# Optimization experiments

Measured on AMD Instinct MI355X. Metric: run time of the kernel, lower is better.

Reference implementation:

```python
import jax, jax.numpy as jnp
import numpy as np

VOCAB, D_MODEL, N_STATE, H_HEADS, LAYERS = 64, 512, 32, 16, 4
EXPAND = 2
D_INNER = EXPAND * D_MODEL          # 1024
P_HEAD = D_INNER // H_HEADS         # 64
CONV_DIM = D_INNER + 2 * N_STATE    # x, B, C share the depthwise conv
K_CONV = 4
D_IN_PROJ = 2 * D_INNER + 2 * N_STATE + H_HEADS  # z, x, B, C, dt
BATCH, SEQ = 4, 1024
EPS = 1e-5


def rmsnorm(x, w):
    return x * jax.lax.rsqrt(jnp.mean(x * x, axis=-1, keepdims=True) + EPS) * w


def silu(x):
    return x * jax.nn.sigmoid(x)


def causal_depthwise_conv(x, w, b):
    # x: [B,L,C], w: [C,K], b: [C]; causal (left) padding, depthwise groups
    xt = jnp.transpose(x, (0, 2, 1))  # [B,C,L]
    out = jax.lax.conv_general_dilated(xt, w[:, None, :], (1,), [(K_CONV - 1, 0)], feature_group_count=w.shape[0])
    return jnp.transpose(out, (0, 2, 1)) + b


def ssd(xh, dt, A, Bm, Cm, Dp):
    # Mamba2 SSD recurrence. xh [B,L,H,P], dt [B,L,H], A [H], Bm/Cm [B,L,N], Dp [H]
    dA = jnp.exp(dt * A)              # decay per (batch, step, head)
    dtx = dt[..., None] * xh          # [B,L,H,P]

    def step(h, inp):
        dA_t, dtx_t, B_t, C_t = inp
        # h: [B,H,P,N]
        h = dA_t[:, :, None, None] * h + dtx_t[..., None] * B_t[:, None, None, :]
        y = jnp.einsum('bhpn,bn->bhp', h, C_t)
        return h, y

    h0 = jnp.zeros((xh.shape[0], H_HEADS, P_HEAD, N_STATE), xh.dtype)
    _, ys = jax.lax.scan(step, h0, (jnp.moveaxis(dA, 1, 0), jnp.moveaxis(dtx, 1, 0), jnp.moveaxis(Bm, 1, 0), jnp.moveaxis(Cm, 1, 0)))
    return jnp.moveaxis(ys, 0, 1) + xh * Dp[None, None, :, None]


def mamba_block(x, norm_w, W_in, b_in, conv_w, conv_b, dt_bias, A_log, Dp, gnorm_w, W_out, b_out):
    res = x
    u = rmsnorm(x, norm_w)
    zxbcdt = u @ W_in + b_in                                # [B,L,D_IN_PROJ]
    z = zxbcdt[..., :D_INNER]
    xBC = zxbcdt[..., D_INNER:D_INNER + CONV_DIM]
    dt = zxbcdt[..., D_INNER + CONV_DIM:]                   # [B,L,H]
    xBC = silu(causal_depthwise_conv(xBC, conv_w, conv_b))
    xc = xBC[..., :D_INNER]
    Bm = xBC[..., D_INNER:D_INNER + N_STATE]
    Cm = xBC[..., D_INNER + N_STATE:]
    dt = jax.nn.softplus(dt + dt_bias)
    xh = xc.reshape(xc.shape[0], xc.shape[1], H_HEADS, P_HEAD)
    y = ssd(xh, dt, -jnp.exp(A_log), Bm, Cm, Dp)
    y = y.reshape(y.shape[0], y.shape[1], D_INNER)
    y = rmsnorm(y * silu(z), gnorm_w)                       # gated RMSNorm
    return res + y @ W_out + b_out


def forward(input_tokens, emb, norm_w, W_in, b_in, conv_w, conv_b, dt_bias, A_log, D_param, gnorm_w, W_out, b_out, head_w, head_b):
    h = emb[input_tokens]
    for i in range(LAYERS):
        h = mamba_block(h, norm_w[i], W_in[i], b_in[i], conv_w[i], conv_b[i], dt_bias[i], A_log[i], D_param[i], gnorm_w[i], W_out[i], b_out[i])
    return h @ head_w + head_b


def setup_inputs() -> dict:
    key = jax.random.key(0)
    ks = jax.random.split(key, 8)
    s = 0.02
    return {
        'input_tokens': jax.random.randint(ks[0], (BATCH, SEQ), 0, VOCAB),
        'emb': jax.random.normal(ks[1], (VOCAB, D_MODEL), jnp.float32) * s,
        'norm_w': jnp.ones((LAYERS, D_MODEL), jnp.float32),
        'W_in': jax.random.normal(ks[2], (LAYERS, D_MODEL, D_IN_PROJ), jnp.float32) * s,
        'b_in': jnp.zeros((LAYERS, D_IN_PROJ), jnp.float32),
        'conv_w': jax.random.normal(ks[3], (LAYERS, CONV_DIM, K_CONV), jnp.float32) * 0.1,
        'conv_b': jnp.zeros((LAYERS, CONV_DIM), jnp.float32),
        'dt_bias': jnp.tile(jnp.log(jnp.expm1(jnp.linspace(0.001, 0.1, H_HEADS, dtype=jnp.float32))), (LAYERS, 1)),
        'A_log': jnp.tile(jnp.log(jnp.arange(1, H_HEADS + 1, dtype=jnp.float32)), (LAYERS, 1)),
        'D_param': jnp.ones((LAYERS, H_HEADS), jnp.float32),
        'gnorm_w': jnp.ones((LAYERS, D_INNER), jnp.float32),
        'W_out': jax.random.normal(ks[4], (LAYERS, D_INNER, D_MODEL), jnp.float32) * s,
        'b_out': jnp.zeros((LAYERS, D_MODEL), jnp.float32),
        'head_w': jax.random.normal(ks[5], (D_MODEL, VOCAB), jnp.float32) * s,
        'head_b': jnp.zeros((VOCAB,), jnp.float32),
    }


def reference(input_tokens, emb, norm_w, W_in, b_in, conv_w, conv_b, dt_bias, A_log, D_param, gnorm_w, W_out, b_out, head_w, head_b):
    return forward(input_tokens, emb, norm_w, W_in, b_in, conv_w, conv_b, dt_bias, A_log, D_param, gnorm_w, W_out, b_out, head_w, head_b)
```

## Files before the change

kernel.cpp:

```cpp
#include <hip/hip_runtime.h>
#include <hip/hip_bf16.h>

#define VOCAB     64
#define D_MODEL   512
#define N_STATE   32
#define H_HEADS   16
#define LAYERS    4
#define D_INNER   1024
#define P_HEAD    64
#define CONV_DIM  1088
#define K_CONV    4
#define D_IN_PROJ 2128
#define NPAD_IN   2176
#define NPAD_HEAD 64
#define BATCH     4
#define SEQ       1024
#define NTOK      (BATCH*SEQ)
#define EPS       1e-5f
#define CL        64
#define NC        (SEQ/CL)
#define PSTR      80

typedef __bf16 bf16x8 __attribute__((ext_vector_type(8)));
typedef float  f32x4  __attribute__((ext_vector_type(4)));

__device__ __forceinline__ float sigmoidf_(float x) { return 1.f / (1.f + __expf(-x)); }
__device__ __forceinline__ float softplusf_(float x) { return (x > 20.f) ? x : log1pf(__expf(x)); }

__device__ __forceinline__ void gload_lds16(const void* g, void* l) {
  __builtin_amdgcn_global_load_lds((const __attribute__((address_space(1))) void*)g,
                                   (__attribute__((address_space(3))) void*)l,
                                   16, 0, 0);
}

__device__ __forceinline__ int xcd_lin() {
  return (blockIdx.x & 7) * ((int)gridDim.x >> 3) + ((int)blockIdx.x >> 3);
}

__global__ __launch_bounds__(256) void prep_kernel(
    const float* __restrict__ W_in, const float* __restrict__ W_out,
    const float* __restrict__ head_w,
    const float* __restrict__ norm_w, const float* __restrict__ gnorm_w,
    __bf16* __restrict__ WtIn, __bf16* __restrict__ WtOut, __bf16* __restrict__ WtHead,
    const int* __restrict__ tok, const float* __restrict__ emb,
    float* __restrict__ h, __bf16* __restrict__ hbf) {
  int b = blockIdx.x;
  if (b >= 6432) {
    int eb = b - 6432;
    int wv = threadIdx.x >> 6, lane = threadIdx.x & 63;
    int tokid = eb * 4 + wv;
    const float* er = emb + (size_t)tok[tokid] * D_MODEL;
    f32x4 v0 = *(const f32x4*)(er + lane * 8);
    f32x4 v1 = *(const f32x4*)(er + lane * 8 + 4);
    float* hr = h + (size_t)tokid * D_MODEL;
    *(f32x4*)(hr + lane * 8) = v0;
    *(f32x4*)(hr + lane * 8 + 4) = v1;
    bf16x8 o8;
    #pragma unroll
    for (int k = 0; k < 4; k++) { o8[k] = (__bf16)v0[k]; o8[4 + k] = (__bf16)v1[k]; }
    *(bf16x8*)(hbf + (size_t)tokid * D_MODEL + lane * 8) = o8;
    return;
  }
  const float* W; const float* fold; __bf16* Wt; int K, N, Npad, bx, by;
  if (b < 4352) {
    int z = b / 1088, r = b % 1088;
    bx = r % 68; by = r / 68;
    W = W_in + (size_t)z * D_MODEL * D_IN_PROJ;
    fold = norm_w + (size_t)z * D_MODEL;
    Wt = WtIn + (size_t)z * NPAD_IN * D_MODEL;
    K = D_MODEL; N = D_IN_PROJ; Npad = NPAD_IN;
  } else if (b < 6400) {
    int r = b - 4352; int z = r / 512; r %= 512;
    bx = r % 16; by = r / 16;
    W = W_out + (size_t)z * D_INNER * D_MODEL;
    fold = gnorm_w + (size_t)z * D_INNER;
    Wt = WtOut + (size_t)z * D_MODEL * D_INNER;
    K = D_INNER; N = D_MODEL; Npad = D_MODEL;
  } else {
    int r = b - 6400;
    bx = r % 2; by = r / 2;
    W = head_w; fold = nullptr; Wt = WtHead;
    K = D_MODEL; N = VOCAB; Npad = NPAD_HEAD;
  }
  __shared__ float T[32][33];
  int n0 = bx * 32, k0 = by * 32;
  int tx = threadIdx.x & 31, ty = threadIdx.x >> 5;
  #pragma unroll
  for (int i = 0; i < 4; i++) {
    int n = n0 + tx;
    T[ty + i * 8][tx] = (n < N) ? W[(size_t)(k0 + ty + i * 8) * N + n] : 0.f;
  }
  __syncthreads();
  float fs = fold ? fold[k0 + tx] : 1.f;
  #pragma unroll
  for (int i = 0; i < 4; i++)
    Wt[(size_t)(n0 + ty + i * 8) * K + k0 + tx] = (__bf16)(T[tx][ty + i * 8] * fs);
}

#define TK 64
__global__ __launch_bounds__(256) void gemm64_kernel(
    const __bf16* __restrict__ A, const __bf16* __restrict__ Bt,
    const float* __restrict__ bias, const float* __restrict__ res,
    float* __restrict__ C, __bf16* __restrict__ Cbf,
    float inv_norm_dim, int nbx, int K, int N, int ldc) {
  __shared__ __bf16 As[3][64 * TK];
  __shared__ __bf16 Bs[3][32 * TK];
  int tid = threadIdx.x;
  int lane = tid & 63, wave = tid >> 6;
  int wm = wave >> 1, wn = wave & 1;
  int q = lane >> 4, l16 = lane & 15;
  int lin = xcd_lin();
  int bx = lin % nbx, by = lin / nbx;
  size_t row0 = (size_t)by * 64;
  int col0 = bx * 32;
  const __bf16* Ab = A + row0 * K;
  const __bf16* Bb = Bt + (size_t)col0 * K;

  auto stage = [&](int buf, int kk) {
    #pragma unroll
    for (int r = 0; r < 2; r++) {
      int lin2 = r * 256 + tid;
      gload_lds16(Ab + (size_t)(lin2 >> 3) * K + kk + (lin2 & 7) * 8, &As[buf][lin2 * 8]);
    }
    {
      int lin2 = tid;
      gload_lds16(Bb + (size_t)(lin2 >> 3) * K + kk + (lin2 & 7) * 8, &Bs[buf][lin2 * 8]);
    }
  };

  f32x4 acc[2];
  acc[0] = (f32x4){0.f, 0.f, 0.f, 0.f};
  acc[1] = (f32x4){0.f, 0.f, 0.f, 0.f};
  float ssqa[2] = {0.f, 0.f};

  int niter = K / TK;
  stage(0, 0);
  if (niter > 1) stage(1, TK);
  int bi = 0;
  for (int i = 0; i < niter; i++) {
    if (i + 2 < niter) {
      stage((bi + 2) % 3, (i + 2) * TK);
      asm volatile("s_waitcnt vmcnt(6)" ::: "memory");
    } else if (i + 1 < niter) {
      asm volatile("s_waitcnt vmcnt(3)" ::: "memory");
    } else {
      asm volatile("s_waitcnt vmcnt(0)" ::: "memory");
    }
    __builtin_amdgcn_s_barrier();
    #pragma unroll
    for (int ks = 0; ks < 2; ks++) {
      bf16x8 af[2], bfv;
      #pragma unroll
      for (int ii = 0; ii < 2; ii++) {
        af[ii] = *(const bf16x8*)(&As[bi][(wm * 32 + ii * 16 + l16) * TK + ks * 32 + q * 8]);
        #pragma unroll
        for (int k = 0; k < 8; k++) { float v = (float)af[ii][k]; ssqa[ii] += v * v; }
      }
      bfv = *(const bf16x8*)(&Bs[bi][(wn * 16 + l16) * TK + ks * 32 + q * 8]);
      #pragma unroll
      for (int ii = 0; ii < 2; ii++)
        acc[ii] = __builtin_amdgcn_mfma_f32_16x16x32_bf16(af[ii], bfv, acc[ii], 0, 0, 0);
    }
    __builtin_amdgcn_s_barrier();
    bi = (bi + 1) % 3;
  }

  #pragma unroll
  for (int i = 0; i < 2; i++) {
    ssqa[i] += __shfl_xor(ssqa[i], 16);
    ssqa[i] += __shfl_xor(ssqa[i], 32);
  }
  #pragma unroll
  for (int i = 0; i < 2; i++) {
    #pragma unroll
    for (int rr = 0; rr < 4; rr++) {
      size_t mrow = row0 + wm * 32 + i * 16 + q * 4 + rr;
      float sq = __shfl(ssqa[i], q * 4 + rr);
      float sc = (inv_norm_dim > 0.f) ? rsqrtf(sq * inv_norm_dim + EPS) : 1.f;
      int col = col0 + wn * 16 + l16;
      if (col < N) {
        size_t off = mrow * (size_t)ldc + col;
        float v = acc[i][rr] * sc + (bias ? bias[col] : 0.f);
        if (res) v += res[off];
        if (C)   C[off] = v;
        if (Cbf) Cbf[off] = (__bf16)v;
      }
    }
  }
}

__global__ __launch_bounds__(256) void gemm_in_kernel(
    const __bf16* __restrict__ A, const __bf16* __restrict__ Bt,
    const float* __restrict__ bias, __bf16* __restrict__ Cbf,
    int nbx, int K, int N, int ldc) {
  __shared__ __bf16 As[64 * TK];
  __shared__ __bf16 Bs[2][128 * TK];
  int tid = threadIdx.x;
  int lane = tid & 63, wave = tid >> 6;
  int wm = wave >> 1, wn = wave & 1;
  int q = lane >> 4, l16 = lane & 15;
  int lin = xcd_lin();
  int bx = lin % nbx, by = lin / nbx;
  size_t row0 = (size_t)by * 64;
  int col0 = bx * 128;
  const __bf16* Ab = A + row0 * K;
  const __bf16* Bb = Bt + (size_t)col0 * K;

  auto stageA = [&](int kk) {
    #pragma unroll
    for (int r = 0; r < 2; r++) {
      int lin2 = r * 256 + tid;
      gload_lds16(Ab + (size_t)(lin2 >> 3) * K + kk + (lin2 & 7) * 8, As + lin2 * 8);
    }
  };
  auto stageB = [&](int buf, int kk) {
    #pragma unroll
    for (int r = 0; r < 4; r++) {
      int lin2 = r * 256 + tid;
      gload_lds16(Bb + (size_t)(lin2 >> 3) * K + kk + (lin2 & 7) * 8, &Bs[buf][lin2 * 8]);
    }
  };

  f32x4 acc[2][4];
  #pragma unroll
  for (int i = 0; i < 2; i++)
    #pragma unroll
    for (int j = 0; j < 4; j++) acc[i][j] = (f32x4){0.f, 0.f, 0.f, 0.f};
  float ssqa[2] = {0.f, 0.f};

  stageA(0);
  stageB(0, 0);
  int cur = 0;
  for (int k0 = 0; k0 < K; k0 += TK) {
    if (k0 + TK < K) {
      stageB(cur ^ 1, k0 + TK);
      asm volatile("s_waitcnt vmcnt(4)" ::: "memory");
    } else {
      asm volatile("s_waitcnt vmcnt(0)" ::: "memory");
    }
    __builtin_amdgcn_s_barrier();
    #pragma unroll
    for (int ks = 0; ks < 2; ks++) {
      bf16x8 af[2], bfv[4];
      #pragma unroll
      for (int i = 0; i < 2; i++) {
        af[i] = *(const bf16x8*)(&As[(wm * 32 + i * 16 + l16) * TK + ks * 32 + q * 8]);
        #pragma unroll
        for (int k = 0; k < 8; k++) { float v = (float)af[i][k]; ssqa[i] += v * v; }
      }
      #pragma unroll
      for (int j = 0; j < 4; j++)
        bfv[j] = *(const bf16x8*)(&Bs[cur][(wn * 64 + j * 16 + l16) * TK + ks * 32 + q * 8]);
      #pragma unroll
      for (int i = 0; i < 2; i++)
        #pragma unroll
        for (int j = 0; j < 4; j++)
          acc[i][j] = __builtin_amdgcn_mfma_f32_16x16x32_bf16(af[i], bfv[j], acc[i][j], 0, 0, 0);
    }
    __builtin_amdgcn_s_barrier();
    if (k0 + TK < K) stageA(k0 + TK);
    cur ^= 1;
  }

  #pragma unroll
  for (int i = 0; i < 2; i++) {
    ssqa[i] += __shfl_xor(ssqa[i], 16);
    ssqa[i] += __shfl_xor(ssqa[i], 32);
  }
  __bf16* Cs = (__bf16*)Bs;
  const int CST = 136;
  float bvj[4];
  #pragma unroll
  for (int j = 0; j < 4; j++) {
    int colj = col0 + wn * 64 + j * 16 + l16;
    bvj[j] = (colj < N) ? bias[colj] : 0.f;
  }
  #pragma unroll
  for (int i = 0; i < 2; i++) {
    #pragma unroll
    for (int rr = 0; rr < 4; rr++) {
      int rloc = wm * 32 + i * 16 + q * 4 + rr;
      float sq = __shfl(ssqa[i], q * 4 + rr);
      float sc = rsqrtf(sq * (1.f / D_MODEL) + EPS);
      #pragma unroll
      for (int j = 0; j < 4; j++)
        Cs[rloc * CST + wn * 64 + j * 16 + l16] = (__bf16)(acc[i][j][rr] * sc + bvj[j]);
    }
  }
  __syncthreads();
  #pragma unroll
  for (int s = 0; s < 2; s++) {
    int idx = s * 256 + tid;
    int row = idx >> 3, c0 = (idx & 7) * 16;
    if (col0 + c0 < N) {
      bf16x8 v0 = *(const bf16x8*)(&Cs[row * CST + c0]);
      bf16x8 v1 = *(const bf16x8*)(&Cs[row * CST + c0 + 8]);
      __bf16* dst = Cbf + (row0 + row) * (size_t)ldc + col0 + c0;
      *(bf16x8*)dst = v0;
      *(bf16x8*)(dst + 8) = v1;
    }
  }
}

__device__ __forceinline__ void wave0_dt_cumsum(
    const __bf16* __restrict__ zxbf, const float* __restrict__ dt_bias,
    int b, int h, int t0, int tid, float* ldt, float* lcs, float* __restrict__ dtcsg) {
  if (tid < 64) {
    float dv = (float)zxbf[((size_t)(b * SEQ + t0 + tid)) * D_IN_PROJ + 2 * D_INNER + 2 * N_STATE + h]
               + dt_bias[h];
    float dtv = softplusf_(dv);
    float cs = dtv;
    #pragma unroll
    for (int off = 1; off < 64; off <<= 1) {
      float o = __shfl_up(cs, off);
      if (tid >= off) cs += o;
    }
    ldt[tid] = dtv;
    lcs[tid] = cs;
    dtcsg[tid] = dtv;
    dtcsg[64 + tid] = cs;
  }
}

__global__ __launch_bounds__(256) void ssd_local_kernel(
    const __bf16* __restrict__ zxbf, const float* __restrict__ conv_w,
    const float* __restrict__ conv_b, const float* __restrict__ dt_bias,
    const float* __restrict__ A_log,
    float* __restrict__ Slocal, float* __restrict__ dAprod,
    __bf16* __restrict__ convx, __bf16* __restrict__ convbc, float* __restrict__ dtcs) {
  int blk = xcd_lin();
  int c = blk % NC;
  int h = (blk / NC) % H_HEADS;
  int b = blk / (NC * H_HEADS);
  int tid = threadIdx.x;
  int lane = tid & 63, wave = tid >> 6;
  int q = lane >> 4, l16 = lane & 15;
  int t0 = c * CL;
  float A = -__expf(A_log[h]);
  __shared__ __bf16 rawbuf[2 * 68 * 64];
  __shared__ __bf16 lxT[64][PSTR];
  __shared__ __bf16 lBTw[32][PSTR];
  __shared__ float ldt[64], lcs[64];
  __bf16* rawx = rawbuf;
  __bf16* rawBC = rawbuf + 68 * 64;
  for (int i = tid; i < 68 * 8; i += 256) {
    int r = i >> 3, c0 = (i & 7) * 8;
    int gr = t0 - 3 + r;
    bf16x8 vx, vbc;
    #pragma unroll
    for (int k = 0; k < 8; k++) { vx[k] = (__bf16)0.f; vbc[k] = (__bf16)0.f; }
    if (gr >= 0) {
      const __bf16* rowp = zxbf + ((size_t)(b * SEQ + gr)) * D_IN_PROJ;
      vx  = *(const bf16x8*)(rowp + D_INNER + h * 64 + c0);
      vbc = *(const bf16x8*)(rowp + 2 * D_INNER + c0);
    }
    *(bf16x8*)(rawx + r * 64 + c0)  = vx;
    *(bf16x8*)(rawBC + r * 64 + c0) = vbc;
  }
  wave0_dt_cumsum(zxbf, dt_bias, b, h, t0, tid, ldt, lcs, dtcs + (size_t)blk * 128);
  __syncthreads();
  float cs63 = lcs[63];
  __bf16* xg  = convx  + (size_t)blk * (64 * PSTR);
  __bf16* bcg = convbc + (size_t)blk * 4096;
  {
    int p = tid & 63;
    const float* w = conv_w + (h * 64 + p) * K_CONV;
    float w0 = w[0], w1 = w[1], w2 = w[2], w3 = w[3];
    float cb = conv_b[h * 64 + p];
    for (int i = tid; i < CL * 64; i += 256) {
      int t = i >> 6;
      float a = cb + w0 * (float)rawx[t * 64 + p] + w1 * (float)rawx[(t + 1) * 64 + p]
                   + w2 * (float)rawx[(t + 2) * 64 + p] + w3 * (float)rawx[(t + 3) * 64 + p];
      lxT[p][t] = (__bf16)(a * sigmoidf_(a));
    }
  }
  {
    int col = tid & 63;
    const float* w = conv_w + (D_INNER + col) * K_CONV;
    float w0 = w[0], w1 = w[1], w2 = w[2], w3 = w[3];
    float cb = conv_b[D_INNER + col];
    for (int i = tid; i < CL * 64; i += 256) {
      int t = i >> 6;
      float a = cb + w0 * (float)rawBC[t * 64 + col] + w1 * (float)rawBC[(t + 1) * 64 + col]
                   + w2 * (float)rawBC[(t + 2) * 64 + col] + w3 * (float)rawBC[(t + 3) * 64 + col];
      float v = a * sigmoidf_(a);
      if (col < 32) {
        bcg[t * 32 + col] = (__bf16)v;
        float wt = ldt[t] * __expf(A * (cs63 - lcs[t]));
        lBTw[col][t] = (__bf16)(v * wt);
      } else {
        bcg[2048 + t * 32 + (col - 32)] = (__bf16)v;
      }
    }
  }
  __syncthreads();
  for (int i = tid; i < (64 * PSTR) / 8; i += 256)
    *(bf16x8*)(xg + i * 8) = *(const bf16x8*)(((const __bf16*)lxT) + i * 8);
  if (c < NC - 1) {
    f32x4 acc0 = (f32x4){0.f,0.f,0.f,0.f}, acc1 = (f32x4){0.f,0.f,0.f,0.f};
    #pragma unroll
    for (int kb = 0; kb < 2; kb++) {
      bf16x8 af = *(const bf16x8*)(&lxT[wave * 16 + l16][kb * 32 + q * 8]);
      bf16x8 b0 = *(const bf16x8*)(&lBTw[l16][kb * 32 + q * 8]);
      bf16x8 b1 = *(const bf16x8*)(&lBTw[l16 + 16][kb * 32 + q * 8]);
      acc0 = __builtin_amdgcn_mfma_f32_16x16x32_bf16(af, b0, acc0, 0, 0, 0);
      acc1 = __builtin_amdgcn_mfma_f32_16x16x32_bf16(af, b1, acc1, 0, 0, 0);
    }
    float* sT = (float*)rawbuf;
    #pragma unroll
    for (int rr = 0; rr < 4; rr++) {
      int p = wave * 16 + q * 4 + rr;
      sT[p * 36 + l16]      = acc0[rr];
      sT[p * 36 + l16 + 16] = acc1[rr];
    }
    int row = tid >> 2, c0 = (tid & 3) * 8;
    f32x4 a = *(const f32x4*)(sT + row * 36 + c0);
    f32x4 b2 = *(const f32x4*)(sT + row * 36 + c0 + 4);
    float* dstp = Slocal + (size_t)blk * 2048 + row * 32 + c0;
    *(f32x4*)dstp = a;
    *(f32x4*)(dstp + 4) = b2;
  }
  if (tid == 0) dAprod[blk] = __expf(A * cs63);
}

__global__ __launch_bounds__(256) void ssd_out_kernel(
    const __bf16* __restrict__ zxbf, const float* __restrict__ A_log,
    const float* __restrict__ Dp,
    const float* __restrict__ Slocal, const float* __restrict__ dAprod,
    const __bf16* __restrict__ convx, const __bf16* __restrict__ convbc,
    const float* __restrict__ dtcs, __bf16* __restrict__ gout) {
  int blk = xcd_lin();
  int c = blk % NC;
  int h = (blk / NC) % H_HEADS;
  int b = blk / (NC * H_HEADS);
  int tid = threadIdx.x;
  int lane = tid & 63, wave = tid >> 6;
  int q = lane >> 4, l16 = lane & 15;
  int t0 = c * CL;
  float A = -__expf(A_log[h]);
  float D = Dp[h];
  __shared__ __bf16 lxT[64][PSTR];
  __shared__ __bf16 pPbuf[64 * PSTR];
  __shared__ __bf16 lBC[2 * 64 * 32];
  __shared__ __bf16 lS[64][32];
  __shared__ float ldt[64], lcs[64];
  const __bf16* xg  = convx  + (size_t)blk * (64 * PSTR);
  const __bf16* bcg = convbc + (size_t)blk * 4096;
  __bf16* lB = lBC;
  __bf16* lC = lBC + 2048;
  for (int i = tid; i < (64 * PSTR) / 8; i += 256)
    gload_lds16(xg + i * 8, ((__bf16*)lxT) + i * 8);
  for (int i = tid; i < 512; i += 256)
    gload_lds16(bcg + i * 8, lBC + i * 8);
  if (tid < 64) {
    const float* dg = dtcs + (size_t)blk * 128;
    ldt[tid] = dg[tid];
    lcs[tid] = dg[64 + tid];
  }
  {
    int p = tid >> 2, n0 = (tid & 3) * 8;
    const float* sl = Slocal + (size_t)(blk - c) * 2048 + p * 32 + n0;
    const float* dab = dAprod + (blk - c);
    float st[8] = {};
    for (int j = 0; j < c; j++) {
      f32x4 a = *(const f32x4*)(sl + (size_t)j * 2048);
      f32x4 bq = *(const f32x4*)(sl + (size_t)j * 2048 + 4);
      float prj = dab[j];
      #pragma unroll
      for (int k = 0; k < 4; k++) { st[k] = prj * st[k] + a[k]; st[4 + k] = prj * st[4 + k] + bq[k]; }
    }
    #pragma unroll
    for (int k = 0; k < 8; k++) lS[p][n0 + k] = (__bf16)st[k];
  }
  __syncthreads();
  bf16x8 afC = *(const bf16x8*)(lC + (wave * 16 + l16) * 32 + q * 8);
  f32x4 accG[4], accI[4], accY[4];
  #pragma unroll
  for (int j = 0; j < 4; j++) {
    accG[j] = (f32x4){0.f,0.f,0.f,0.f};
    accI[j] = (f32x4){0.f,0.f,0.f,0.f};
    accY[j] = (f32x4){0.f,0.f,0.f,0.f};
  }
  #pragma unroll
  for (int j = 0; j < 4; j++) {
    bf16x8 bf = *(const bf16x8*)(lB + (l16 + 16 * j) * 32 + q * 8);
    accG[j] = __builtin_amdgcn_mfma_f32_16x16x32_bf16(afC, bf, accG[j], 0, 0, 0);
  }
  #pragma unroll
  for (int j = 0; j < 4; j++) {
    bf16x8 bf = *(const bf16x8*)(&lS[l16 + 16 * j][q * 8]);
    accI[j] = __builtin_amdgcn_mfma_f32_16x16x32_bf16(afC, bf, accI[j], 0, 0, 0);
  }
  __bf16* pP = pPbuf + wave * 16 * PSTR;
  #pragma unroll
  for (int j = 0; j < 4; j++) {
    int s = l16 + 16 * j;
    float css = lcs[s], dts = ldt[s];
    #pragma unroll
    for (int rr = 0; rr < 4; rr++) {
      int tl = q * 4 + rr;
      int t = wave * 16 + tl;
      float val = accG[j][rr] * __expf(A * (lcs[t] - css)) * dts;
      if (s == t) val += D;
      if (s > t) val = 0.f;
      pP[tl * PSTR + s] = (__bf16)val;
    }
  }
  #pragma unroll
  for (int kb = 0; kb < 2; kb++) {
    bf16x8 afP = *(const bf16x8*)(pP + l16 * PSTR + kb * 32 + q * 8);
    #pragma unroll
    for (int j = 0; j < 4; j++) {
      bf16x8 bf = *(const bf16x8*)(&lxT[l16 + 16 * j][kb * 32 + q * 8]);
      accY[j] = __builtin_amdgcn_mfma_f32_16x16x32_bf16(afP, bf, accY[j], 0, 0, 0);
    }
  }
  __syncthreads();
  __bf16* yT = pPbuf;
  #pragma unroll
  for (int rr = 0; rr < 4; rr++) {
    int t = wave * 16 + q * 4 + rr;
    float cumt = __expf(A * lcs[t]);
    #pragma unroll
    for (int j = 0; j < 4; j++) {
      int p = l16 + 16 * j;
      yT[t * 72 + p] = (__bf16)(accY[j][rr] + cumt * accI[j][rr]);
    }
  }
  {
    int row = tid >> 2, col0 = (tid & 3) * 16;
    bf16x8 y0 = *(const bf16x8*)(yT + row * 72 + col0);
    bf16x8 y1 = *(const bf16x8*)(yT + row * 72 + col0 + 8);
    const __bf16* zrow = zxbf + ((size_t)(b * SEQ + t0 + row)) * D_IN_PROJ + h * 64 + col0;
    bf16x8 z0 = *(const bf16x8*)zrow;
    bf16x8 z1 = *(const bf16x8*)(zrow + 8);
    bf16x8 g0, g1;
    #pragma unroll
    for (int k = 0; k < 8; k++) {
      float zz = (float)z0[k];
      g0[k] = (__bf16)((float)y0[k] * zz * sigmoidf_(zz));
    }
    #pragma unroll
    for (int k = 0; k < 8; k++) {
      float zz = (float)z1[k];
      g1[k] = (__bf16)((float)y1[k] * zz * sigmoidf_(zz));
    }
    __bf16* grow = gout + ((size_t)(b * SEQ + t0 + row)) * D_INNER + h * 64 + col0;
    *(bf16x8*)grow = g0;
    *(bf16x8*)(grow + 8) = g1;
  }
}

extern "C" void kernel_launch(void* const* d_in, const int* in_sizes, int n_in,
                              void* d_out, int out_size, void* d_ws, size_t ws_size,
                              hipStream_t stream) {
  const int*   tok     = (const int*)  d_in[0];
  const float* emb     = (const float*)d_in[1];
  const float* norm_w  = (const float*)d_in[2];
  const float* W_in    = (const float*)d_in[3];
  const float* b_in    = (const float*)d_in[4];
  const float* conv_w  = (const float*)d_in[5];
  const float* conv_b  = (const float*)d_in[6];
  const float* dt_bias = (const float*)d_in[7];
  const float* A_log   = (const float*)d_in[8];
  const float* D_par   = (const float*)d_in[9];
  const float* gnorm_w = (const float*)d_in[10];
  const float* W_out   = (const float*)d_in[11];
  const float* b_out   = (const float*)d_in[12];
  const float* head_w  = (const float*)d_in[13];
  const float* head_b  = (const float*)d_in[14];
  float* out = (float*)d_out;

  char* p = (char*)d_ws;
  auto alloc = [&](size_t bytes) { void* r = (void*)p; p += (bytes + 255) & ~(size_t)255; return r; };
  float*  h      = (float*) alloc((size_t)NTOK * D_MODEL * 4);
  float*  slocal = (float*) alloc((size_t)BATCH * H_HEADS * NC * P_HEAD * N_STATE * 4);
  float*  daprod = (float*) alloc((size_t)BATCH * H_HEADS * NC * 4);
  float*  dtcs   = (float*) alloc((size_t)1024 * 128 * 4);
  __bf16* convx  = (__bf16*)alloc((size_t)1024 * 64 * PSTR * 2);
  __bf16* convbc = (__bf16*)alloc((size_t)1024 * 4096 * 2);
  __bf16* zxbf   = (__bf16*)alloc((size_t)NTOK * D_IN_PROJ * 2);
  __bf16* gbf    = (__bf16*)alloc((size_t)NTOK * D_INNER * 2);
  __bf16* hbf    = (__bf16*)alloc((size_t)NTOK * D_MODEL * 2);
  __bf16* WtIn   = (__bf16*)alloc((size_t)LAYERS * NPAD_IN * D_MODEL * 2);
  __bf16* WtOut  = (__bf16*)alloc((size_t)LAYERS * D_MODEL * D_INNER * 2);
  __bf16* WtHead = (__bf16*)alloc((size_t)NPAD_HEAD * D_MODEL * 2);

  prep_kernel<<<6432 + NTOK / 4, 256, 0, stream>>>(
      W_in, W_out, head_w, norm_w, gnorm_w, WtIn, WtOut, WtHead,
      tok, emb, h, hbf);

  for (int l = 0; l < LAYERS; l++) {
    gemm_in_kernel<<<1088, 256, 0, stream>>>(
        hbf, WtIn + (size_t)l * NPAD_IN * D_MODEL, b_in + (size_t)l * D_IN_PROJ,
        zxbf, NPAD_IN / 128, D_MODEL, D_IN_PROJ, D_IN_PROJ);

    ssd_local_kernel<<<BATCH * H_HEADS * NC, 256, 0, stream>>>(
        zxbf, conv_w + (size_t)l * CONV_DIM * K_CONV, conv_b + (size_t)l * CONV_DIM,
        dt_bias + (size_t)l * H_HEADS, A_log + (size_t)l * H_HEADS, slocal, daprod,
        convx, convbc, dtcs);
    ssd_out_kernel<<<BATCH * H_HEADS * NC, 256, 0, stream>>>(
        zxbf, A_log + (size_t)l * H_HEADS, D_par + (size_t)l * H_HEADS,
        slocal, daprod, convx, convbc, dtcs, gbf);

    gemm64_kernel<<<1024, 256, 0, stream>>>(
        gbf, WtOut + (size_t)l * D_MODEL * D_INNER, b_out + (size_t)l * D_MODEL, h,
        h, hbf, 1.f / D_INNER, D_MODEL / 32, D_INNER, D_MODEL, D_MODEL);
  }

  gemm64_kernel<<<128, 256, 0, stream>>>(
      hbf, WtHead, head_b, nullptr, out, nullptr, 0.f, NPAD_HEAD / 32, D_MODEL, VOCAB, VOCAB);
}
```

Before: 431.9 us.

## Triple-buffer input-projection GEMM with smaller K tile and prefetch depth two

```diff
diff --git a/kernel.cpp b/kernel.cpp
--- a/kernel.cpp
+++ b/kernel.cpp
@@ -189,12 +189,13 @@
   }
 }
 
+#define TKI 32
 __global__ __launch_bounds__(256) void gemm_in_kernel(
     const __bf16* __restrict__ A, const __bf16* __restrict__ Bt,
     const float* __restrict__ bias, __bf16* __restrict__ Cbf,
     int nbx, int K, int N, int ldc) {
-  __shared__ __bf16 As[64 * TK];
-  __shared__ __bf16 Bs[2][128 * TK];
+  __shared__ __bf16 As[3][64 * TKI];
+  __shared__ __bf16 Bs[3][128 * TKI];
   int tid = threadIdx.x;
   int lane = tid & 63, wave = tid >> 6;
   int wm = wave >> 1, wn = wave & 1;
@@ -206,18 +207,14 @@
   const __bf16* Ab = A + row0 * K;
   const __bf16* Bb = Bt + (size_t)col0 * K;
 
-  auto stageA = [&](int kk) {
+  auto stage = [&](int buf, int kk) {
+    {
+      gload_lds16(Ab + (size_t)(tid >> 2) * K + kk + (tid & 3) * 8, &As[buf][tid * 8]);
+    }
     #pragma unroll
     for (int r = 0; r < 2; r++) {
       int lin2 = r * 256 + tid;
-      gload_lds16(Ab + (size_t)(lin2 >> 3) * K + kk + (lin2 & 7) * 8, As + lin2 * 8);
-    }
-  };
-  auto stageB = [&](int buf, int kk) {
-    #pragma unroll
-    for (int r = 0; r < 4; r++) {
-      int lin2 = r * 256 + tid;
-      gload_lds16(Bb + (size_t)(lin2 >> 3) * K + kk + (lin2 & 7) * 8, &Bs[buf][lin2 * 8]);
+      gload_lds16(Bb + (size_t)(lin2 >> 2) * K + kk + (lin2 & 3) * 8, &Bs[buf][lin2 * 8]);
     }
   };
 
@@ -228,38 +225,39 @@
     for (int j = 0; j < 4; j++) acc[i][j] = (f32x4){0.f, 0.f, 0.f, 0.f};
   float ssqa[2] = {0.f, 0.f};
 
-  stageA(0);
-  stageB(0, 0);
-  int cur = 0;
-  for (int k0 = 0; k0 < K; k0 += TK) {
-    if (k0 + TK < K) {
-      stageB(cur ^ 1, k0 + TK);
-      asm volatile("s_waitcnt vmcnt(4)" ::: "memory");
+  int niter = K / TKI;
+  stage(0, 0);
+  stage(1, TKI);
+  int bi = 0;
+  for (int i = 0; i < niter; i++) {
+    if (i + 2 < niter) {
+      stage((bi + 2) % 3, (i + 2) * TKI);
+      asm volatile("s_waitcnt vmcnt(6)" ::: "memory");
+    } else if (i + 1 < niter) {
+      asm volatile("s_waitcnt vmcnt(3)" ::: "memory");
     } else {
       asm volatile("s_waitcnt vmcnt(0)" ::: "memory");
     }
     __builtin_amdgcn_s_barrier();
-    #pragma unroll
-    for (int ks = 0; ks < 2; ks++) {
+    {
       bf16x8 af[2], bfv[4];
       #pragma unroll
-      for (int i = 0; i < 2; i++) {
-        af[i] = *(const bf16x8*)(&As[(wm * 32 + i * 16 + l16) * TK + ks * 32 + q * 8]);
+      for (int ii = 0; ii < 2; ii++) {
+        af[ii] = *(const bf16x8*)(&As[bi][(wm * 32 + ii * 16 + l16) * TKI + q * 8]);
         #pragma unroll
-        for (int k = 0; k < 8; k++) { float v = (float)af[i][k]; ssqa[i] += v * v; }
+        for (int k = 0; k < 8; k++) { float v = (float)af[ii][k]; ssqa[ii] += v * v; }
       }
       #pragma unroll
       for (int j = 0; j < 4; j++)
-        bfv[j] = *(const bf16x8*)(&Bs[cur][(wn * 64 + j * 16 + l16) * TK + ks * 32 + q * 8]);
+        bfv[j] = *(const bf16x8*)(&Bs[bi][(wn * 64 + j * 16 + l16) * TKI + q * 8]);
       #pragma unroll
-      for (int i = 0; i < 2; i++)
+      for (int ii = 0; ii < 2; ii++)
         #pragma unroll
         for (int j = 0; j < 4; j++)
-          acc[i][j] = __builtin_amdgcn_mfma_f32_16x16x32_bf16(af[i], bfv[j], acc[i][j], 0, 0, 0);
+          acc[ii][j] = __builtin_amdgcn_mfma_f32_16x16x32_bf16(af[ii], bfv[j], acc[ii][j], 0, 0, 0);
     }
     __builtin_amdgcn_s_barrier();
-    if (k0 + TK < K) stageA(k0 + TK);
-    cur ^= 1;
+    bi = (bi + 1) % 3;
   }
 
   #pragma unroll
```

Result: no change. 436.7 us (+1.1%).
